# Optimization experiments

Hardware: AMD Instinct MI355X
Metric: run time of the kernel (lower is better)

## Reference

```python
import jax, jax.numpy as jnp
import numpy as np

B, S, T, H, NH, NL = 16, 128, 64, 128, 8, 4
DH = H // NH
FF = 2 * H
SCALE = 1.0 / float(np.sqrt(DH))


def _ln(x, s, b):
    m = x.mean(-1, keepdims=True)
    v = ((x - m) ** 2).mean(-1, keepdims=True)
    return (x - m) * jax.lax.rsqrt(v + 1e-5) * s + b


def _block(x, mask, p):
    Wq, bq, Wk, bk, Wv, bv, Wo, bo, s1, c1, W1, d1, W2, d2, s2, c2 = p
    N, L, _ = x.shape
    q = (x @ Wq + bq).reshape(N, L, NH, DH)
    k = (x @ Wk + bk).reshape(N, L, NH, DH)
    v = (x @ Wv + bv).reshape(N, L, NH, DH)
    scores = jnp.einsum('nqhd,nkhd->nhqk', q, k) * SCALE
    scores = jnp.where(mask[:, None, :, :], scores, -1e9)
    a = jax.nn.softmax(scores, axis=-1)
    o = jnp.einsum('nhqk,nkhd->nqhd', a, v).reshape(N, L, H)
    x = _ln(x + o @ Wo + bo, s1, c1)
    h = jax.nn.relu(x @ W1 + d1)
    return _ln(x + h @ W2 + d2, s2, c2)


def setup_inputs():
    key = jax.random.key(0)
    ks = jax.random.split(key, 16)
    g = lambda k, shape: jax.random.normal(k, shape, jnp.float32) * 0.02
    return {
        'polylines': jax.random.normal(ks[0], (B, S, T, H), jnp.float32),
        'lengths': jax.random.randint(ks[1], (B, S), 0, T + 1),
        'proj_w': g(ks[2], (H, H)), 'proj_b': jnp.zeros((H,), jnp.float32),
        'proj_ln_s': jnp.ones((H,), jnp.float32), 'proj_ln_b': jnp.zeros((H,), jnp.float32),
        'pos_emb': g(ks[3], (1, T, H)),
        'Wq': g(ks[4], (NL, H, H)), 'bq': jnp.zeros((NL, H), jnp.float32),
        'Wk': g(ks[5], (NL, H, H)), 'bk': jnp.zeros((NL, H), jnp.float32),
        'Wv': g(ks[6], (NL, H, H)), 'bv': jnp.zeros((NL, H), jnp.float32),
        'Wo': g(ks[7], (NL, H, H)), 'bo': jnp.zeros((NL, H), jnp.float32),
        'ln1_s': jnp.ones((NL, H), jnp.float32), 'ln1_b': jnp.zeros((NL, H), jnp.float32),
        'W1': g(ks[8], (NL, H, FF)), 'b1': jnp.zeros((NL, FF), jnp.float32),
        'W2': g(ks[9], (NL, FF, H)), 'b2': jnp.zeros((NL, H), jnp.float32),
        'ln2_s': jnp.ones((NL, H), jnp.float32), 'ln2_b': jnp.zeros((NL, H), jnp.float32),
    }


def reference(polylines, lengths, proj_w, proj_b, proj_ln_s, proj_ln_b, pos_emb,
              Wq, bq, Wk, bk, Wv, bv, Wo, bo, ln1_s, ln1_b, W1, b1, W2, b2, ln2_s, ln2_b):
    # valid[b,s,t] = t < lengths[b,s]; lengths==0 -> polyline absent (fully padded)
    valid = jnp.arange(T)[None, None, :] < lengths[:, :, None]  # [B,S,T]
    x = jnp.where(valid[..., None], polylines, -1.0)            # -1 pad as in np.pad(constant_values=-1)
    # mask_temporal[b,s] = outer(valid[b,s], valid[b,s])
    mask_t = (valid[:, :, :, None] & valid[:, :, None, :]).reshape(B * S, T, T)
    # mask_spatial[b,t] = outer(valid[b,:,t], valid[b,:,t])
    vs = jnp.transpose(valid, (0, 2, 1))                        # [B,T,S]
    mask_s = (vs[:, :, :, None] & vs[:, :, None, :]).reshape(B * T, S, S)

    x = x.reshape(B * S, T, H)
    x = jax.nn.relu(_ln(x @ proj_w + proj_b, proj_ln_s, proj_ln_b))  # MLP: Linear->LN->ReLU
    x = x + pos_emb[:, :T, :]

    mask = mask_t
    for i in range(NL):
        if i == NL // 2:
            # switch from temporal to spatial attention: [B*S,T,H] -> [B*T,S,H]
            x = x.reshape(B, S, T, H).transpose(0, 2, 1, 3).reshape(B * T, S, H)
            mask = mask_s
        p = (Wq[i], bq[i], Wk[i], bk[i], Wv[i], bv[i], Wo[i], bo[i],
             ln1_s[i], ln1_b[i], W1[i], b1[i], W2[i], b2[i], ln2_s[i], ln2_b[i])
        x = _block(x, mask, p)
    # faithful to original final reshape (treats [B*T,S,H] buffer as [B,S,T,H])
    return x.reshape(B, S, T, H)[:, 0, :]
```

## Files before the change

kernel.cpp:

```cpp
#include <hip/hip_runtime.h>

typedef short short8 __attribute__((ext_vector_type(8)));
typedef short short4_t __attribute__((ext_vector_type(4)));
typedef float floatx4 __attribute__((ext_vector_type(4)));
typedef unsigned short ushort_t;

#define B_ 16
#define S_ 128
#define T_ 64
#define H_ 128
#define FF_ 256
#define SCALEQK 0.25f

#define OFFP 0
#define OFFQ(l) (16384 + (l) * 65536)
#define OFFK(l) (OFFQ(l) + 16384)
#define OFFV(l) (OFFQ(l) + 32768)
#define OFFO(l) (OFFQ(l) + 49152)
#define OFFW1(l) (278528 + (l) * 65536)
#define OFFW2(l) (OFFW1(l) + 32768)

__device__ __forceinline__ float b2f(ushort_t u) {
    union { unsigned int i; float f; } x; x.i = ((unsigned int)u) << 16; return x.f;
}
__device__ __forceinline__ ushort_t f2b(float f) {
    union { float f; unsigned int i; } x; x.f = f;
    unsigned int r = x.i + 0x7fffu + ((x.i >> 16) & 1u);
    return (ushort_t)(r >> 16);
}
__device__ __forceinline__ int pack2b(float a, float b) {
    return (int)f2b(a) | ((int)f2b(b) << 16);
}

struct WtEnt { const float* src; int N; int K; int nclog2; int dstoff; };
struct WtArgs { WtEnt e[25]; };

__global__ __launch_bounds__(256) void wt_kernel(WtArgs a, ushort_t* __restrict__ dst) {
    WtEnt ent = a.e[blockIdx.x];
    const int tiles_c = ent.N >> 5;
    const int nt = (ent.K >> 5) * tiles_c;
    const int t = blockIdx.y;
    if (t >= nt) return;
    const int tc = t & (tiles_c - 1);
    const int tr = t >> ent.nclog2;
    __shared__ float ld[32 * 33];
    const int tid = threadIdx.x;
#pragma unroll
    for (int i = 0; i < 4; ++i) {
        int e = tid + i * 256;
        int rr = e >> 5, cc = e & 31;
        ld[rr * 33 + cc] = ent.src[(tr * 32 + rr) * ent.N + tc * 32 + cc];
    }
    __syncthreads();
    ushort_t* d = dst + ent.dstoff;
#pragma unroll
    for (int i = 0; i < 4; ++i) {
        int e = tid + i * 256;
        int rr = e >> 5, cc = e & 31;
        d[(tc * 32 + rr) * ent.K + tr * 32 + cc] = f2b(ld[cc * 33 + rr]);
    }
}

template<int RT, int CT, int KK>
__device__ __forceinline__ void mm_g(const ushort_t* aL, int sa,
                                     const ushort_t* __restrict__ wT,
                                     int colbase, int lane, floatx4 (&acc)[RT][CT]) {
    const int l15 = lane & 15, lq8 = (lane >> 4) * 8;
#pragma unroll
    for (int r = 0; r < RT; ++r)
#pragma unroll
        for (int c = 0; c < CT; ++c) acc[r][c] = (floatx4){0.f, 0.f, 0.f, 0.f};
#pragma unroll
    for (int k0 = 0; k0 < KK; k0 += 32) {
        short8 b[CT];
#pragma unroll
        for (int c = 0; c < CT; ++c)
            b[c] = *(const short8*)&wT[(colbase + c * 16 + l15) * KK + k0 + lq8];
#pragma unroll
        for (int r = 0; r < RT; ++r) {
            short8 a = *(const short8*)&aL[(r * 16 + l15) * sa + k0 + lq8];
#pragma unroll
            for (int c = 0; c < CT; ++c)
                acc[r][c] = __builtin_amdgcn_mfma_f32_16x16x32_bf16(a, b[c], acc[r][c], 0, 0, 0);
        }
    }
}

template<int RT, int CT>
__device__ __forceinline__ void add_bias(floatx4 (&acc)[RT][CT], const float* b,
                                         int colbase, int l15) {
#pragma unroll
    for (int c = 0; c < CT; ++c) {
        float bc = b[colbase + c * 16 + l15];
#pragma unroll
        for (int r = 0; r < RT; ++r)
#pragma unroll
            for (int g = 0; g < 4; ++g) acc[r][c][g] += bc;
    }
}

template<int RT, int CT>
__device__ __forceinline__ void add_resid_reg(floatx4 (&acc)[RT][CT],
                                              const float (&res)[RT][CT][4]) {
#pragma unroll
    for (int r = 0; r < RT; ++r)
#pragma unroll
        for (int c = 0; c < CT; ++c)
#pragma unroll
            for (int g = 0; g < 4; ++g) acc[r][c][g] += res[r][c][g];
}
template<int RT, int CT>
__device__ __forceinline__ void save_resid(float (&res)[RT][CT][4],
                                           const floatx4 (&acc)[RT][CT]) {
#pragma unroll
    for (int r = 0; r < RT; ++r)
#pragma unroll
        for (int c = 0; c < CT; ++c)
#pragma unroll
            for (int g = 0; g < 4; ++g) res[r][c][g] = acc[r][c][g];
}

template<int RT, int CT>
__device__ __forceinline__ void st_n(const floatx4 (&acc)[RT][CT], ushort_t* dst, int stride,
                                     int colbase, int l15, int lq) {
#pragma unroll
    for (int r = 0; r < RT; ++r)
#pragma unroll
        for (int g = 0; g < 4; ++g) {
            int row = r * 16 + lq * 4 + g;
#pragma unroll
            for (int c = 0; c < CT; ++c)
                dst[row * stride + colbase + c * 16 + l15] = f2b(acc[r][c][g]);
        }
}

template<int RT, int CT>
__device__ __forceinline__ void st_t(const floatx4 (&acc)[RT][CT], ushort_t* dst, int stride,
                                     int colbase, int l15, int lq) {
#pragma unroll
    for (int r = 0; r < RT; ++r)
#pragma unroll
        for (int c = 0; c < CT; ++c) {
            int d = colbase + c * 16 + l15;
            short4_t p;
#pragma unroll
            for (int g = 0; g < 4; ++g) p[g] = (short)f2b(acc[r][c][g]);
            *(short4_t*)&dst[d * stride + r * 16 + lq * 4] = p;
        }
}

template<int RT, int CT>
__device__ __forceinline__ void ln_norm(floatx4 (&acc)[RT][CT], float* redL,
                                        const float* lns, const float* lnb,
                                        int colbase, int l15, int lq, int wv) {
#pragma unroll
    for (int r = 0; r < RT; ++r)
#pragma unroll
        for (int g = 0; g < 4; ++g) {
            float s = 0.f, q = 0.f;
#pragma unroll
            for (int c = 0; c < CT; ++c) { float v = acc[r][c][g]; s += v; q += v * v; }
            s += __shfl_xor(s, 1); s += __shfl_xor(s, 2); s += __shfl_xor(s, 4); s += __shfl_xor(s, 8);
            q += __shfl_xor(q, 1); q += __shfl_xor(q, 2); q += __shfl_xor(q, 4); q += __shfl_xor(q, 8);
            if (l15 == 0) {
                int row = r * 16 + lq * 4 + g;
                redL[row * 8 + wv] = s;
                redL[row * 8 + 4 + wv] = q;
            }
        }
    __syncthreads();
#pragma unroll
    for (int r = 0; r < RT; ++r)
#pragma unroll
        for (int g = 0; g < 4; ++g) {
            int row = r * 16 + lq * 4 + g;
            float4 S = *(float4*)&redL[row * 8];
            float4 Q = *(float4*)&redL[row * 8 + 4];
            float mean = (S.x + S.y + S.z + S.w) * (1.f / 128.f);
            float var = (Q.x + Q.y + Q.z + Q.w) * (1.f / 128.f) - mean * mean;
            float rstd = rsqrtf(var + 1e-5f);
#pragma unroll
            for (int c = 0; c < CT; ++c) {
                int col = colbase + c * 16 + l15;
                acc[r][c][g] = (acc[r][c][g] - mean) * rstd * lns[col] + lnb[col];
            }
        }
}

template<int JT>
__device__ __forceinline__ void softmax_pack(floatx4 (&st)[JT], bool iv, unsigned jm,
                                             int (&px)[JT][2]) {
    float ev[JT][4];
    float mx = -3.0e38f;
#pragma unroll
    for (int jt = 0; jt < JT; ++jt)
#pragma unroll
        for (int g = 0; g < 4; ++g) {
            bool ok = iv && ((jm >> (jt * 4 + g)) & 1u);
            float s = ok ? st[jt][g] * SCALEQK : -1e9f;
            ev[jt][g] = s; mx = fmaxf(mx, s);
        }
    mx = fmaxf(mx, __shfl_xor(mx, 16)); mx = fmaxf(mx, __shfl_xor(mx, 32));
    float sum = 0.f;
#pragma unroll
    for (int jt = 0; jt < JT; ++jt)
#pragma unroll
        for (int g = 0; g < 4; ++g) { float e = __expf(ev[jt][g] - mx); ev[jt][g] = e; sum += e; }
    sum += __shfl_xor(sum, 16); sum += __shfl_xor(sum, 32);
    float inv = 1.f / sum;
#pragma unroll
    for (int jt = 0; jt < JT; ++jt) {
        px[jt][0] = pack2b(ev[jt][0] * inv, ev[jt][1] * inv);
        px[jt][1] = pack2b(ev[jt][2] * inv, ev[jt][3] * inv);
    }
}

__device__ __forceinline__ short8 pfrag(const int (*px)[2], int jc, int lq, int l15) {
    const int jA = (lq & 1) * 32 + l15;
    int a0 = __shfl(px[jc * 2][0], jA);
    int a1 = __shfl(px[jc * 2][1], jA);
    int a2 = __shfl(px[jc * 2][0], jA + 16);
    int a3 = __shfl(px[jc * 2][1], jA + 16);
    int b0 = __shfl(px[jc * 2 + 1][0], jA);
    int b1 = __shfl(px[jc * 2 + 1][1], jA);
    int b2 = __shfl(px[jc * 2 + 1][0], jA + 16);
    int b3 = __shfl(px[jc * 2 + 1][1], jA + 16);
    const bool t = (lq >> 1) != 0;
    union { int4 i; short8 s; } u;
    u.i = make_int4(t ? b0 : a0, t ? b1 : a1, t ? b2 : a2, t ? b3 : a3);
    return u.s;
}
__device__ __forceinline__ short8 vfrag(const ushort_t* vT, int stride, int row, int off) {
    int2 a = *(const int2*)&vT[row * stride + off];
    int2 b = *(const int2*)&vT[row * stride + off + 4];
    union { int4 i; short8 s; } u;
    u.i = make_int4(a.x, a.y, b.x, b.y);
    return u.s;
}

__global__ __launch_bounds__(256, 2) void k1_mega(
    const float* __restrict__ poly, const int* __restrict__ lens,
    const ushort_t* __restrict__ wt,
    const float* __restrict__ projb, const float* __restrict__ pls,
    const float* __restrict__ plb, const float* __restrict__ pos,
    const float* __restrict__ bq0, const float* __restrict__ bk0,
    const float* __restrict__ bv0, const float* __restrict__ bo0,
    const float* __restrict__ l1s0, const float* __restrict__ l1b0,
    const float* __restrict__ b10, const float* __restrict__ b20,
    const float* __restrict__ l2s0, const float* __restrict__ l2b0,
    const float* __restrict__ bq1, const float* __restrict__ bk1,
    const float* __restrict__ bv1,
    ushort_t* __restrict__ o1, float* __restrict__ xr0f)
{
    __shared__ ushort_t pool[34816];
    __shared__ float redL[512];
    __shared__ float psL[8 * 68];
    __shared__ float q1L[128];
    ushort_t* xL = pool;
    ushort_t* qL = pool + 8704;
    ushort_t* kL = pool + 17408;
    ushort_t* vT = pool + 26112;
    ushort_t* hL = pool + 17408;

    const int tid = threadIdx.x, lane = tid & 63, wv = tid >> 6;
    const int l15 = lane & 15, lq = lane >> 4;
    const int g = blockIdx.x;
    const int len = lens[g];

    {
        const float* pg = poly + (size_t)g * 8192;
#pragma unroll
        for (int it = 0; it < 8; ++it) {
            int e4 = (tid + it * 256) * 4;
            int row = e4 >> 7, col = e4 & 127;
            float4 f = *(const float4*)(pg + e4);
            if (row >= len) { f.x = -1.f; f.y = -1.f; f.z = -1.f; f.w = -1.f; }
            short4_t u;
            u[0] = (short)f2b(f.x); u[1] = (short)f2b(f.y);
            u[2] = (short)f2b(f.z); u[3] = (short)f2b(f.w);
            *(short4_t*)&xL[row * 136 + col] = u;
        }
    }
    __syncthreads();

    floatx4 a2[4][2];
    float xre[4][2][4];

    mm_g<4, 2, 128>(xL, 136, wt + OFFP, wv * 32, lane, a2);
    add_bias<4, 2>(a2, projb, wv * 32, l15);
    ln_norm<4, 2>(a2, redL, pls, plb, wv * 32, l15, lq, wv);
    __syncthreads();
#pragma unroll
    for (int r = 0; r < 4; ++r)
#pragma unroll
        for (int gg = 0; gg < 4; ++gg) {
            int row = r * 16 + lq * 4 + gg;
#pragma unroll
            for (int c = 0; c < 2; ++c) {
                int col = wv * 32 + c * 16 + l15;
                float v = fmaxf(a2[r][c][gg], 0.f) + pos[row * 128 + col];
                xre[r][c][gg] = v;
                xL[row * 136 + col] = f2b(v);
            }
        }
    __syncthreads();

    mm_g<4, 2, 128>(xL, 136, wt + OFFQ(0), wv * 32, lane, a2);
    add_bias<4, 2>(a2, bq0, wv * 32, l15);
    st_n<4, 2>(a2, qL, 136, wv * 32, l15, lq);
    mm_g<4, 2, 128>(xL, 136, wt + OFFK(0), wv * 32, lane, a2);
    add_bias<4, 2>(a2, bk0, wv * 32, l15);
    st_n<4, 2>(a2, kL, 136, wv * 32, l15, lq);
    mm_g<4, 2, 128>(xL, 136, wt + OFFV(0), wv * 32, lane, a2);
    add_bias<4, 2>(a2, bv0, wv * 32, l15);
    st_t<4, 2>(a2, vT, 68, wv * 32, l15, lq);
    __syncthreads();

    {
        const int iRow = wv * 16 + l15;
        const bool iv = iRow < len;
        unsigned jm = 0;
#pragma unroll
        for (int jt = 0; jt < 4; ++jt)
#pragma unroll
            for (int gg = 0; gg < 4; ++gg)
                if (jt * 16 + lq * 4 + gg < len) jm |= (1u << (jt * 4 + gg));
        for (int h = 0; h < 8; ++h) {
            const int hc = h * 16;
            short8 z8 = {0, 0, 0, 0, 0, 0, 0, 0};
            short8 bqf = z8;
            if (lq < 2) bqf = *(const short8*)&qL[iRow * 136 + hc + lq * 8];
            floatx4 st[4];
#pragma unroll
            for (int jt = 0; jt < 4; ++jt) {
                short8 ak = z8;
                if (lq < 2) ak = *(const short8*)&kL[(jt * 16 + l15) * 136 + hc + lq * 8];
                floatx4 zz = {0.f, 0.f, 0.f, 0.f};
                st[jt] = __builtin_amdgcn_mfma_f32_16x16x32_bf16(ak, bqf, zz, 0, 0, 0);
            }
            int px[4][2];
            softmax_pack<4>(st, iv, jm, px);
            floatx4 ao = {0.f, 0.f, 0.f, 0.f};
#pragma unroll
            for (int jc = 0; jc < 2; ++jc) {
                short8 av = vfrag(vT, 68, hc + l15, jc * 32 + lq * 8);
                short8 bp = pfrag(px, jc, lq, l15);
                ao = __builtin_amdgcn_mfma_f32_16x16x32_bf16(av, bp, ao, 0, 0, 0);
            }
            short4_t w;
#pragma unroll
            for (int gg = 0; gg < 4; ++gg) w[gg] = (short)f2b(ao[gg]);
            *(short4_t*)&qL[iRow * 136 + hc + lq * 4] = w;
        }
    }
    __syncthreads();

    mm_g<4, 2, 128>(qL, 136, wt + OFFO(0), wv * 32, lane, a2);
    add_bias<4, 2>(a2, bo0, wv * 32, l15);
    add_resid_reg<4, 2>(a2, xre);
    ln_norm<4, 2>(a2, redL, l1s0, l1b0, wv * 32, l15, lq, wv);
    save_resid<4, 2>(xre, a2);
    st_n<4, 2>(a2, xL, 136, wv * 32, l15, lq);
    __syncthreads();

    {
        floatx4 a4[4][4];
        mm_g<4, 4, 128>(xL, 136, wt + OFFW1(0), wv * 64, lane, a4);
        add_bias<4, 4>(a4, b10, wv * 64, l15);
#pragma unroll
        for (int r = 0; r < 4; ++r)
#pragma unroll
            for (int c = 0; c < 4; ++c)
#pragma unroll
                for (int gg = 0; gg < 4; ++gg) a4[r][c][gg] = fmaxf(a4[r][c][gg], 0.f);
        st_n<4, 4>(a4, hL, 272, wv * 64, l15, lq);
    }
    __syncthreads();

    mm_g<4, 2, 256>(hL, 272, wt + OFFW2(0), wv * 32, lane, a2);
    add_bias<4, 2>(a2, b20, wv * 32, l15);
    add_resid_reg<4, 2>(a2, xre);
    ln_norm<4, 2>(a2, redL, l2s0, l2b0, wv * 32, l15, lq, wv);
    save_resid<4, 2>(xre, a2);
    st_n<4, 2>(a2, xL, 136, wv * 32, l15, lq);
    if (lq == 0) {
#pragma unroll
        for (int c = 0; c < 2; ++c)
            xr0f[(size_t)g * 128 + wv * 32 + c * 16 + l15] = a2[0][c][0];
    }
    __syncthreads();

    mm_g<4, 2, 128>(xL, 136, wt + OFFK(1), wv * 32, lane, a2);
    add_bias<4, 2>(a2, bk1, wv * 32, l15);
    st_n<4, 2>(a2, kL, 136, wv * 32, l15, lq);
    mm_g<4, 2, 128>(xL, 136, wt + OFFV(1), wv * 32, lane, a2);
    add_bias<4, 2>(a2, bv1, wv * 32, l15);
    st_t<4, 2>(a2, vT, 68, wv * 32, l15, lq);
    if (tid < 128) {
        int d = tid;
        float a = bq1[d];
        const ushort_t* wq = wt + OFFQ(1) + d * 128;
#pragma unroll 4
        for (int j0 = 0; j0 < 128; j0 += 8) {
            short8 w8 = *(const short8*)&wq[j0];
            short8 x8 = *(const short8*)&xL[j0];
#pragma unroll
            for (int q = 0; q < 8; ++q)
                a = fmaf(b2f((ushort_t)x8[q]), b2f((ushort_t)w8[q]), a);
        }
        q1L[d] = a;
    }
    __syncthreads();

    {
        int h = tid >> 5, jj = tid & 31;
        int hc = h * 16;
        float s[2];
#pragma unroll
        for (int half = 0; half < 2; ++half) {
            int j = jj + half * 32;
            float a = 0.f;
            short8 k0v = *(const short8*)&kL[j * 136 + hc];
            short8 k1v = *(const short8*)&kL[j * 136 + hc + 8];
#pragma unroll
            for (int q = 0; q < 8; ++q) {
                a = fmaf(q1L[hc + q], b2f((ushort_t)k0v[q]), a);
                a = fmaf(q1L[hc + 8 + q], b2f((ushort_t)k1v[q]), a);
            }
            s[half] = (j < len) ? a * SCALEQK : -1e9f;
        }
        float mx = fmaxf(s[0], s[1]);
#pragma unroll
        for (int d = 1; d < 32; d <<= 1) mx = fmaxf(mx, __shfl_xor(mx, d));
        float e0 = __expf(s[0] - mx), e1 = __expf(s[1] - mx);
        float sum = e0 + e1;
#pragma unroll
        for (int d = 1; d < 32; d <<= 1) sum += __shfl_xor(sum, d);
        float inv = 1.f / sum;
        psL[h * 68 + jj] = e0 * inv;
        psL[h * 68 + jj + 32] = e1 * inv;
    }
    __syncthreads();
    if (tid < 128) {
        int h = tid >> 4, d = tid & 15, hc = h * 16;
        float a = 0.f;
#pragma unroll 4
        for (int j0 = 0; j0 < 64; j0 += 4) {
            float4 p4 = *(const float4*)&psL[h * 68 + j0];
            short4_t v4 = *(const short4_t*)&vT[(hc + d) * 68 + j0];
            a += p4.x * b2f((ushort_t)v4[0]) + p4.y * b2f((ushort_t)v4[1])
               + p4.z * b2f((ushort_t)v4[2]) + p4.w * b2f((ushort_t)v4[3]);
        }
        o1[(size_t)g * 128 + hc + d] = f2b(a);
    }
}

__global__ __launch_bounds__(256, 1) void k2_tail(
    const int* __restrict__ lens, const ushort_t* __restrict__ wt,
    const ushort_t* __restrict__ o1, const float* __restrict__ xr0f,
    const float* __restrict__ bq, const float* __restrict__ bk,
    const float* __restrict__ bv, const float* __restrict__ bo,
    const float* __restrict__ l1s, const float* __restrict__ l1b,
    const float* __restrict__ b1, const float* __restrict__ b2,
    const float* __restrict__ l2s, const float* __restrict__ l2b,
    float* __restrict__ outp)
{
    __shared__ ushort_t pool[69632];
    __shared__ float redL[1024];
    __shared__ int vld[128];
    ushort_t* yL = pool;
    ushort_t* qL = pool + 17408;
    ushort_t* kL = pool + 34816;
    ushort_t* vT = pool + 52224;
    ushort_t* hL = pool + 34816;

    const int tid = threadIdx.x, lane = tid & 63, wv = tid >> 6;
    const int l15 = lane & 15, lq = lane >> 4;
    const int b = blockIdx.x;

    if (tid < 128) vld[tid] = (lens[b * 128 + tid] > 0) ? 1 : 0;
#pragma unroll
    for (int it = 0; it < 8; ++it) {
        int e = tid + it * 256;
        int row = e >> 4, cg = e & 15;
        *(short8*)&kL[row * 136 + cg * 8] =
            *(const short8*)&o1[((size_t)b * 128 + row) * 128 + cg * 8];
    }
    __syncthreads();

    floatx4 a2[8][2];
    float yre[8][2][4];

    mm_g<8, 2, 128>(kL, 136, wt + OFFO(1), wv * 32, lane, a2);
    add_bias<8, 2>(a2, bo + 128, wv * 32, l15);
#pragma unroll
    for (int r = 0; r < 8; ++r)
#pragma unroll
        for (int gg = 0; gg < 4; ++gg) {
            int row = r * 16 + lq * 4 + gg;
#pragma unroll
            for (int c = 0; c < 2; ++c)
                a2[r][c][gg] += xr0f[((size_t)b * 128 + row) * 128 + wv * 32 + c * 16 + l15];
        }
    ln_norm<8, 2>(a2, redL, l1s + 128, l1b + 128, wv * 32, l15, lq, wv);
    save_resid<8, 2>(yre, a2);
    st_n<8, 2>(a2, yL, 136, wv * 32, l15, lq);
    __syncthreads();
    {
        floatx4 a4[8][4];
        mm_g<8, 4, 128>(yL, 136, wt + OFFW1(1), wv * 64, lane, a4);
        add_bias<8, 4>(a4, b1 + FF_, wv * 64, l15);
#pragma unroll
        for (int r = 0; r < 8; ++r)
#pragma unroll
            for (int c = 0; c < 4; ++c)
#pragma unroll
                for (int gg = 0; gg < 4; ++gg) a4[r][c][gg] = fmaxf(a4[r][c][gg], 0.f);
        st_n<8, 4>(a4, hL, 272, wv * 64, l15, lq);
    }
    __syncthreads();
    mm_g<8, 2, 256>(hL, 272, wt + OFFW2(1), wv * 32, lane, a2);
    add_bias<8, 2>(a2, b2 + 128, wv * 32, l15);
    add_resid_reg<8, 2>(a2, yre);
    ln_norm<8, 2>(a2, redL, l2s + 128, l2b + 128, wv * 32, l15, lq, wv);
    save_resid<8, 2>(yre, a2);
    st_n<8, 2>(a2, yL, 136, wv * 32, l15, lq);
    __syncthreads();

    unsigned jm = 0;
#pragma unroll
    for (int jt = 0; jt < 8; ++jt)
#pragma unroll
        for (int gg = 0; gg < 4; ++gg)
            if (vld[jt * 16 + lq * 4 + gg]) jm |= (1u << (jt * 4 + gg));
    const int i0 = wv * 32 + l15, i1 = i0 + 16;
    const bool iv0 = vld[i0] != 0, iv1 = vld[i1] != 0;

    for (int l = 2; l < 4; ++l) {
        mm_g<8, 2, 128>(yL, 136, wt + OFFQ(l), wv * 32, lane, a2);
        add_bias<8, 2>(a2, bq + l * 128, wv * 32, l15);
        st_n<8, 2>(a2, qL, 136, wv * 32, l15, lq);
        mm_g<8, 2, 128>(yL, 136, wt + OFFK(l), wv * 32, lane, a2);
        add_bias<8, 2>(a2, bk + l * 128, wv * 32, l15);
        st_n<8, 2>(a2, kL, 136, wv * 32, l15, lq);
        mm_g<8, 2, 128>(yL, 136, wt + OFFV(l), wv * 32, lane, a2);
        add_bias<8, 2>(a2, bv + l * 128, wv * 32, l15);
        st_t<8, 2>(a2, vT, 136, wv * 32, l15, lq);
        __syncthreads();
        for (int h = 0; h < 8; ++h) {
            const int hc = h * 16;
            short8 z8 = {0, 0, 0, 0, 0, 0, 0, 0};
            short8 bqa = z8, bqb = z8;
            if (lq < 2) {
                bqa = *(const short8*)&qL[i0 * 136 + hc + lq * 8];
                bqb = *(const short8*)&qL[i1 * 136 + hc + lq * 8];
            }
            floatx4 s0[8], s1[8];
#pragma unroll
            for (int jt = 0; jt < 8; ++jt) {
                short8 ak = z8;
                if (lq < 2) ak = *(const short8*)&kL[(jt * 16 + l15) * 136 + hc + lq * 8];
                floatx4 zz = {0.f, 0.f, 0.f, 0.f};
                s0[jt] = __builtin_amdgcn_mfma_f32_16x16x32_bf16(ak, bqa, zz, 0, 0, 0);
                s1[jt] = __builtin_amdgcn_mfma_f32_16x16x32_bf16(ak, bqb, zz, 0, 0, 0);
            }
            int px0[8][2], px1[8][2];
            softmax_pack<8>(s0, iv0, jm, px0);
            softmax_pack<8>(s1, iv1, jm, px1);
            floatx4 o0 = {0.f, 0.f, 0.f, 0.f}, o1a = {0.f, 0.f, 0.f, 0.f};
#pragma unroll
            for (int jc = 0; jc < 4; ++jc) {
                short8 av = vfrag(vT, 136, hc + l15, jc * 32 + lq * 8);
                o0 = __builtin_amdgcn_mfma_f32_16x16x32_bf16(av, pfrag(px0, jc, lq, l15), o0, 0, 0, 0);
                o1a = __builtin_amdgcn_mfma_f32_16x16x32_bf16(av, pfrag(px1, jc, lq, l15), o1a, 0, 0, 0);
            }
            short4_t w0, w1;
#pragma unroll
            for (int gg = 0; gg < 4; ++gg) { w0[gg] = (short)f2b(o0[gg]); w1[gg] = (short)f2b(o1a[gg]); }
            *(short4_t*)&qL[i0 * 136 + hc + lq * 4] = w0;
            *(short4_t*)&qL[i1 * 136 + hc + lq * 4] = w1;
        }
        __syncthreads();
        mm_g<8, 2, 128>(qL, 136, wt + OFFO(l), wv * 32, lane, a2);
        add_bias<8, 2>(a2, bo + l * 128, wv * 32, l15);
        add_resid_reg<8, 2>(a2, yre);
        ln_norm<8, 2>(a2, redL, l1s + l * 128, l1b + l * 128, wv * 32, l15, lq, wv);
        save_resid<8, 2>(yre, a2);
        st_n<8, 2>(a2, yL, 136, wv * 32, l15, lq);
        __syncthreads();
        {
            floatx4 a4[8][4];
            mm_g<8, 4, 128>(yL, 136, wt + OFFW1(l), wv * 64, lane, a4);
            add_bias<8, 4>(a4, b1 + l * FF_, wv * 64, l15);
#pragma unroll
            for (int r = 0; r < 8; ++r)
#pragma unroll
                for (int c = 0; c < 4; ++c)
#pragma unroll
                    for (int gg = 0; gg < 4; ++gg) a4[r][c][gg] = fmaxf(a4[r][c][gg], 0.f);
            st_n<8, 4>(a4, hL, 272, wv * 64, l15, lq);
        }
        __syncthreads();
        mm_g<8, 2, 256>(hL, 272, wt + OFFW2(l), wv * 32, lane, a2);
        add_bias<8, 2>(a2, b2 + l * 128, wv * 32, l15);
        add_resid_reg<8, 2>(a2, yre);
        ln_norm<8, 2>(a2, redL, l2s + l * 128, l2b + l * 128, wv * 32, l15, lq, wv);
        if (l == 3) {
#pragma unroll
            for (int r = 0; r < 4; ++r)
#pragma unroll
                for (int gg = 0; gg < 4; ++gg) {
                    int row = r * 16 + lq * 4 + gg;
#pragma unroll
                    for (int c = 0; c < 2; ++c)
                        outp[(size_t)b * 8192 + row * 128 + wv * 32 + c * 16 + l15] = a2[r][c][gg];
                }
        } else {
            save_resid<8, 2>(yre, a2);
            st_n<8, 2>(a2, yL, 136, wv * 32, l15, lq);
        }
        __syncthreads();
    }
}

extern "C" void kernel_launch(void* const* d_in, const int* in_sizes, int n_in,
                              void* d_out, int out_size, void* d_ws, size_t ws_size,
                              hipStream_t stream)
{
    const float* poly   = (const float*)d_in[0];
    const int*   lens   = (const int*)d_in[1];
    const float* proj_w = (const float*)d_in[2];
    const float* proj_b = (const float*)d_in[3];
    const float* pls    = (const float*)d_in[4];
    const float* plb    = (const float*)d_in[5];
    const float* pos    = (const float*)d_in[6];
    const float* Wq = (const float*)d_in[7];
    const float* bq = (const float*)d_in[8];
    const float* Wk = (const float*)d_in[9];
    const float* bk = (const float*)d_in[10];
    const float* Wv = (const float*)d_in[11];
    const float* bv = (const float*)d_in[12];
    const float* Wo = (const float*)d_in[13];
    const float* bo = (const float*)d_in[14];
    const float* l1s = (const float*)d_in[15];
    const float* l1b = (const float*)d_in[16];
    const float* W1 = (const float*)d_in[17];
    const float* b1 = (const float*)d_in[18];
    const float* W2 = (const float*)d_in[19];
    const float* b2 = (const float*)d_in[20];
    const float* l2s = (const float*)d_in[21];
    const float* l2b = (const float*)d_in[22];
    float* outp = (float*)d_out;

    char* base = (char*)d_ws;
    ushort_t* wt    = (ushort_t*)base;
    ushort_t* o1buf = (ushort_t*)(base + 1081344);
    float* xr0f     = (float*)(base + 1605632);

    const int HH = H_ * H_, HF = H_ * FF_;
    WtArgs wa;
    wa.e[0] = {proj_w, 128, 128, 2, OFFP};
    for (int l = 0; l < 4; ++l) {
        wa.e[1 + l * 4 + 0] = {Wq + l * HH, 128, 128, 2, OFFQ(l)};
        wa.e[1 + l * 4 + 1] = {Wk + l * HH, 128, 128, 2, OFFK(l)};
        wa.e[1 + l * 4 + 2] = {Wv + l * HH, 128, 128, 2, OFFV(l)};
        wa.e[1 + l * 4 + 3] = {Wo + l * HH, 128, 128, 2, OFFO(l)};
    }
    for (int l = 0; l < 4; ++l) {
        wa.e[17 + l * 2 + 0] = {W1 + l * HF, 256, 128, 3, OFFW1(l)};
        wa.e[17 + l * 2 + 1] = {W2 + l * HF, 128, 256, 2, OFFW2(l)};
    }
    wt_kernel<<<dim3(25, 32), 256, 0, stream>>>(wa, wt);

    k1_mega<<<dim3(2048), 256, 0, stream>>>(
        poly, lens, wt,
        proj_b, pls, plb, pos,
        bq, bk, bv, bo, l1s, l1b, b1, b2, l2s, l2b,
        bq + H_, bk + H_, bv + H_,
        o1buf, xr0f);

    k2_tail<<<dim3(16), 256, 0, stream>>>(
        lens, wt, o1buf, xr0f,
        bq, bk, bv, bo, l1s, l1b, b1, b2, l2s, l2b,
        outp);
}
```

Baseline: 471.6 us.

## Move layer-1 Wo/LN/FFN tail from 16-block k2 into 2048-block k1

The layer-1 output projection, first layernorm, FFN and second layernorm for the single needed row (t=0) are now computed per polyline inside k1_mega using scalar dot products over bf16 weights, and written as fp32 to a buffer. k2_tail, which runs only 16 blocks, no longer performs these three matmuls and two layernorms over 128 rows; it just loads the finished activations. This spreads serial tail work across many blocks, at the cost of extra per-block latency and weight reads in k1.

```diff
diff --git a/kernel.cpp b/kernel.cpp
--- a/kernel.cpp
+++ b/kernel.cpp
@@ -249,13 +249,17 @@
     const float* __restrict__ b10, const float* __restrict__ b20,
     const float* __restrict__ l2s0, const float* __restrict__ l2b0,
     const float* __restrict__ bq1, const float* __restrict__ bk1,
-    const float* __restrict__ bv1,
-    ushort_t* __restrict__ o1, float* __restrict__ xr0f)
+    const float* __restrict__ bv1, const float* __restrict__ bo1,
+    const float* __restrict__ l1s1, const float* __restrict__ l1b1,
+    const float* __restrict__ b11, const float* __restrict__ b21,
+    const float* __restrict__ l2s1, const float* __restrict__ l2b1,
+    float* __restrict__ ybuf)
 {
     __shared__ ushort_t pool[34816];
     __shared__ float redL[512];
     __shared__ float psL[8 * 68];
     __shared__ float q1L[128];
+    __shared__ float x0L[128];
     ushort_t* xL = pool;
     ushort_t* qL = pool + 8704;
     ushort_t* kL = pool + 17408;
@@ -264,11 +268,11 @@
 
     const int tid = threadIdx.x, lane = tid & 63, wv = tid >> 6;
     const int l15 = lane & 15, lq = lane >> 4;
-    const int g = blockIdx.x;
-    const int len = lens[g];
+    const int gid = blockIdx.x;
+    const int len = lens[gid];
 
     {
-        const float* pg = poly + (size_t)g * 8192;
+        const float* pg = poly + (size_t)gid * 8192;
 #pragma unroll
         for (int it = 0; it < 8; ++it) {
             int e4 = (tid + it * 256) * 4;
@@ -386,7 +390,7 @@
     if (lq == 0) {
 #pragma unroll
         for (int c = 0; c < 2; ++c)
-            xr0f[(size_t)g * 128 + wv * 32 + c * 16 + l15] = a2[0][c][0];
+            x0L[wv * 32 + c * 16 + l15] = a2[0][c][0];
     }
     __syncthreads();
 
@@ -451,13 +455,85 @@
             a += p4.x * b2f((ushort_t)v4[0]) + p4.y * b2f((ushort_t)v4[1])
                + p4.z * b2f((ushort_t)v4[2]) + p4.w * b2f((ushort_t)v4[3]);
         }
-        o1[(size_t)g * 128 + hc + d] = f2b(a);
+        q1L[tid] = a;
+    }
+    __syncthreads();
+
+    float accv = 0.f;
+    if (tid < 128) {
+        accv = bo1[tid] + x0L[tid];
+        const ushort_t* wrow = wt + OFFO(1) + tid * 128;
+#pragma unroll 4
+        for (int j0 = 0; j0 < 128; j0 += 8) {
+            short8 w8 = *(const short8*)&wrow[j0];
+#pragma unroll
+            for (int q = 0; q < 8; ++q)
+                accv = fmaf(q1L[j0 + q], b2f((ushort_t)w8[q]), accv);
+        }
+    }
+    {
+        float s = accv, q = accv * accv;
+        s += __shfl_xor(s, 1); s += __shfl_xor(s, 2); s += __shfl_xor(s, 4);
+        s += __shfl_xor(s, 8); s += __shfl_xor(s, 16); s += __shfl_xor(s, 32);
+        q += __shfl_xor(q, 1); q += __shfl_xor(q, 2); q += __shfl_xor(q, 4);
+        q += __shfl_xor(q, 8); q += __shfl_xor(q, 16); q += __shfl_xor(q, 32);
+        if (lane == 0 && wv < 2) { redL[wv] = s; redL[2 + wv] = q; }
+    }
+    __syncthreads();
+    if (tid < 128) {
+        float s = redL[0] + redL[1], q = redL[2] + redL[3];
+        float mean = s * (1.f / 128.f);
+        float rstd = rsqrtf(q * (1.f / 128.f) - mean * mean + 1e-5f);
+        q1L[tid] = (accv - mean) * rstd * l1s1[tid] + l1b1[tid];
+    }
+    __syncthreads();
+
+    {
+        float hh = b11[tid];
+        const ushort_t* wrow = wt + OFFW1(1) + tid * 128;
+#pragma unroll 4
+        for (int j0 = 0; j0 < 128; j0 += 8) {
+            short8 w8 = *(const short8*)&wrow[j0];
+#pragma unroll
+            for (int q = 0; q < 8; ++q)
+                hh = fmaf(q1L[j0 + q], b2f((ushort_t)w8[q]), hh);
+        }
+        psL[tid] = fmaxf(hh, 0.f);
+    }
+    __syncthreads();
+
+    accv = 0.f;
+    if (tid < 128) {
+        accv = b21[tid] + q1L[tid];
+        const ushort_t* wrow = wt + OFFW2(1) + tid * 256;
+#pragma unroll 4
+        for (int j0 = 0; j0 < 256; j0 += 8) {
+            short8 w8 = *(const short8*)&wrow[j0];
+#pragma unroll
+            for (int q = 0; q < 8; ++q)
+                accv = fmaf(psL[j0 + q], b2f((ushort_t)w8[q]), accv);
+        }
+    }
+    {
+        float s = accv, q = accv * accv;
+        s += __shfl_xor(s, 1); s += __shfl_xor(s, 2); s += __shfl_xor(s, 4);
+        s += __shfl_xor(s, 8); s += __shfl_xor(s, 16); s += __shfl_xor(s, 32);
+        q += __shfl_xor(q, 1); q += __shfl_xor(q, 2); q += __shfl_xor(q, 4);
+        q += __shfl_xor(q, 8); q += __shfl_xor(q, 16); q += __shfl_xor(q, 32);
+        if (lane == 0 && wv < 2) { redL[4 + wv] = s; redL[6 + wv] = q; }
+    }
+    __syncthreads();
+    if (tid < 128) {
+        float s = redL[4] + redL[5], q = redL[6] + redL[7];
+        float mean = s * (1.f / 128.f);
+        float rstd = rsqrtf(q * (1.f / 128.f) - mean * mean + 1e-5f);
+        ybuf[(size_t)gid * 128 + tid] = (accv - mean) * rstd * l2s1[tid] + l2b1[tid];
     }
 }
 
 __global__ __launch_bounds__(256, 1) void k2_tail(
     const int* __restrict__ lens, const ushort_t* __restrict__ wt,
-    const ushort_t* __restrict__ o1, const float* __restrict__ xr0f,
+    const float* __restrict__ ybuf,
     const float* __restrict__ bq, const float* __restrict__ bk,
     const float* __restrict__ bv, const float* __restrict__ bo,
     const float* __restrict__ l1s, const float* __restrict__ l1b,
@@ -479,52 +555,23 @@
     const int b = blockIdx.x;
 
     if (tid < 128) vld[tid] = (lens[b * 128 + tid] > 0) ? 1 : 0;
-#pragma unroll
-    for (int it = 0; it < 8; ++it) {
-        int e = tid + it * 256;
-        int row = e >> 4, cg = e & 15;
-        *(short8*)&kL[row * 136 + cg * 8] =
-            *(const short8*)&o1[((size_t)b * 128 + row) * 128 + cg * 8];
-    }
-    __syncthreads();
 
     floatx4 a2[8][2];
     float yre[8][2][4];
 
-    mm_g<8, 2, 128>(kL, 136, wt + OFFO(1), wv * 32, lane, a2);
-    add_bias<8, 2>(a2, bo + 128, wv * 32, l15);
 #pragma unroll
     for (int r = 0; r < 8; ++r)
 #pragma unroll
         for (int gg = 0; gg < 4; ++gg) {
             int row = r * 16 + lq * 4 + gg;
 #pragma unroll
-            for (int c = 0; c < 2; ++c)
-                a2[r][c][gg] += xr0f[((size_t)b * 128 + row) * 128 + wv * 32 + c * 16 + l15];
-        }
-    ln_norm<8, 2>(a2, redL, l1s + 128, l1b + 128, wv * 32, l15, lq, wv);
-    save_resid<8, 2>(yre, a2);
-    st_n<8, 2>(a2, yL, 136, wv * 32, l15, lq);
-    __syncthreads();
-    {
-        floatx4 a4[8][4];
-        mm_g<8, 4, 128>(yL, 136, wt + OFFW1(1), wv * 64, lane, a4);
-        add_bias<8, 4>(a4, b1 + FF_, wv * 64, l15);
-#pragma unroll
-        for (int r = 0; r < 8; ++r)
-#pragma unroll
-            for (int c = 0; c < 4; ++c)
-#pragma unroll
-                for (int gg = 0; gg < 4; ++gg) a4[r][c][gg] = fmaxf(a4[r][c][gg], 0.f);
-        st_n<8, 4>(a4, hL, 272, wv * 64, l15, lq);
-    }
-    __syncthreads();
-    mm_g<8, 2, 256>(hL, 272, wt + OFFW2(1), wv * 32, lane, a2);
-    add_bias<8, 2>(a2, b2 + 128, wv * 32, l15);
-    add_resid_reg<8, 2>(a2, yre);
-    ln_norm<8, 2>(a2, redL, l2s + 128, l2b + 128, wv * 32, l15, lq, wv);
-    save_resid<8, 2>(yre, a2);
-    st_n<8, 2>(a2, yL, 136, wv * 32, l15, lq);
+            for (int c = 0; c < 2; ++c) {
+                int col = wv * 32 + c * 16 + l15;
+                float v = ybuf[((size_t)b * 128 + row) * 128 + col];
+                yre[r][c][gg] = v;
+                yL[row * 136 + col] = f2b(v);
+            }
+        }
     __syncthreads();
 
     unsigned jm = 0;
@@ -653,9 +700,8 @@
     float* outp = (float*)d_out;
 
     char* base = (char*)d_ws;
-    ushort_t* wt    = (ushort_t*)base;
-    ushort_t* o1buf = (ushort_t*)(base + 1081344);
-    float* xr0f     = (float*)(base + 1605632);
+    ushort_t* wt = (ushort_t*)base;
+    float* ybuf  = (float*)(base + 1081344);
 
     const int HH = H_ * H_, HF = H_ * FF_;
     WtArgs wa;
@@ -676,11 +722,12 @@
         poly, lens, wt,
         proj_b, pls, plb, pos,
         bq, bk, bv, bo, l1s, l1b, b1, b2, l2s, l2b,
-        bq + H_, bk + H_, bv + H_,
-        o1buf, xr0f);
+        bq + H_, bk + H_, bv + H_, bo + H_,
+        l1s + H_, l1b + H_, b1 + FF_, b2 + H_, l2s + H_, l2b + H_,
+        ybuf);
 
     k2_tail<<<dim3(16), 256, 0, stream>>>(
-        lens, wt, o1buf, xr0f,
+        lens, wt, ybuf,
         bq, bk, bv, bo, l1s, l1b, b1, b2, l2s, l2b,
         outp);
 }
```

New measurement: 486.7 us. +3.2%, slower.

## Double k2_tail block to 512 threads, one head per wave in attention

Applied to the files above, without the earlier changes.

The tail kernel runs only 16 blocks, so it now uses 8 waves per block instead of 4. Each wave owns 16 output columns in the projections and FFN, and exactly one attention head. The LayerNorm reduction is templated on wave count so cross-wave partial sums cover 8 waves. This is meant to cut the latency of the serial tail kernel, at the cost of more registers per block and more LDS reduction traffic.

```diff
diff --git a/kernel.cpp b/kernel.cpp
--- a/kernel.cpp
+++ b/kernel.cpp
@@ -149,7 +149,7 @@
         }
 }
 
-template<int RT, int CT>
+template<int RT, int CT, int NW>
 __device__ __forceinline__ void ln_norm(floatx4 (&acc)[RT][CT], float* redL,
                                         const float* lns, const float* lnb,
                                         int colbase, int l15, int lq, int wv) {
@@ -164,8 +164,8 @@
             q += __shfl_xor(q, 1); q += __shfl_xor(q, 2); q += __shfl_xor(q, 4); q += __shfl_xor(q, 8);
             if (l15 == 0) {
                 int row = r * 16 + lq * 4 + g;
-                redL[row * 8 + wv] = s;
-                redL[row * 8 + 4 + wv] = q;
+                redL[row * 2 * NW + wv] = s;
+                redL[row * 2 * NW + NW + wv] = q;
             }
         }
     __syncthreads();
@@ -174,10 +174,16 @@
 #pragma unroll
         for (int g = 0; g < 4; ++g) {
             int row = r * 16 + lq * 4 + g;
-            float4 S = *(float4*)&redL[row * 8];
-            float4 Q = *(float4*)&redL[row * 8 + 4];
-            float mean = (S.x + S.y + S.z + S.w) * (1.f / 128.f);
-            float var = (Q.x + Q.y + Q.z + Q.w) * (1.f / 128.f) - mean * mean;
+            float s = 0.f, q = 0.f;
+#pragma unroll
+            for (int w8 = 0; w8 < NW; w8 += 4) {
+                float4 S = *(float4*)&redL[row * 2 * NW + w8];
+                float4 Q = *(float4*)&redL[row * 2 * NW + NW + w8];
+                s += S.x + S.y + S.z + S.w;
+                q += Q.x + Q.y + Q.z + Q.w;
+            }
+            float mean = s * (1.f / 128.f);
+            float var = q * (1.f / 128.f) - mean * mean;
             float rstd = rsqrtf(var + 1e-5f);
 #pragma unroll
             for (int c = 0; c < CT; ++c) {
@@ -264,11 +270,11 @@
 
     const int tid = threadIdx.x, lane = tid & 63, wv = tid >> 6;
     const int l15 = lane & 15, lq = lane >> 4;
-    const int g = blockIdx.x;
-    const int len = lens[g];
+    const int gid = blockIdx.x;
+    const int len = lens[gid];
 
     {
-        const float* pg = poly + (size_t)g * 8192;
+        const float* pg = poly + (size_t)gid * 8192;
 #pragma unroll
         for (int it = 0; it < 8; ++it) {
             int e4 = (tid + it * 256) * 4;
@@ -288,7 +294,7 @@
 
     mm_g<4, 2, 128>(xL, 136, wt + OFFP, wv * 32, lane, a2);
     add_bias<4, 2>(a2, projb, wv * 32, l15);
-    ln_norm<4, 2>(a2, redL, pls, plb, wv * 32, l15, lq, wv);
+    ln_norm<4, 2, 4>(a2, redL, pls, plb, wv * 32, l15, lq, wv);
     __syncthreads();
 #pragma unroll
     for (int r = 0; r < 4; ++r)
@@ -358,7 +364,7 @@
     mm_g<4, 2, 128>(qL, 136, wt + OFFO(0), wv * 32, lane, a2);
     add_bias<4, 2>(a2, bo0, wv * 32, l15);
     add_resid_reg<4, 2>(a2, xre);
-    ln_norm<4, 2>(a2, redL, l1s0, l1b0, wv * 32, l15, lq, wv);
+    ln_norm<4, 2, 4>(a2, redL, l1s0, l1b0, wv * 32, l15, lq, wv);
     save_resid<4, 2>(xre, a2);
     st_n<4, 2>(a2, xL, 136, wv * 32, l15, lq);
     __syncthreads();
@@ -380,13 +386,13 @@
     mm_g<4, 2, 256>(hL, 272, wt + OFFW2(0), wv * 32, lane, a2);
     add_bias<4, 2>(a2, b20, wv * 32, l15);
     add_resid_reg<4, 2>(a2, xre);
-    ln_norm<4, 2>(a2, redL, l2s0, l2b0, wv * 32, l15, lq, wv);
+    ln_norm<4, 2, 4>(a2, redL, l2s0, l2b0, wv * 32, l15, lq, wv);
     save_resid<4, 2>(xre, a2);
     st_n<4, 2>(a2, xL, 136, wv * 32, l15, lq);
     if (lq == 0) {
 #pragma unroll
         for (int c = 0; c < 2; ++c)
-            xr0f[(size_t)g * 128 + wv * 32 + c * 16 + l15] = a2[0][c][0];
+            xr0f[(size_t)gid * 128 + wv * 32 + c * 16 + l15] = a2[0][c][0];
     }
     __syncthreads();
 
@@ -451,11 +457,11 @@
             a += p4.x * b2f((ushort_t)v4[0]) + p4.y * b2f((ushort_t)v4[1])
                + p4.z * b2f((ushort_t)v4[2]) + p4.w * b2f((ushort_t)v4[3]);
         }
-        o1[(size_t)g * 128 + hc + d] = f2b(a);
-    }
-}
-
-__global__ __launch_bounds__(256, 1) void k2_tail(
+        o1[(size_t)gid * 128 + hc + d] = f2b(a);
+    }
+}
+
+__global__ __launch_bounds__(512, 1) void k2_tail(
     const int* __restrict__ lens, const ushort_t* __restrict__ wt,
     const ushort_t* __restrict__ o1, const float* __restrict__ xr0f,
     const float* __restrict__ bq, const float* __restrict__ bk,
@@ -466,7 +472,7 @@
     float* __restrict__ outp)
 {
     __shared__ ushort_t pool[69632];
-    __shared__ float redL[1024];
+    __shared__ float redL[2048];
     __shared__ int vld[128];
     ushort_t* yL = pool;
     ushort_t* qL = pool + 17408;
@@ -477,54 +483,54 @@
     const int tid = threadIdx.x, lane = tid & 63, wv = tid >> 6;
     const int l15 = lane & 15, lq = lane >> 4;
     const int b = blockIdx.x;
+    const int cb1 = wv * 16;
+    const int cb2 = wv * 32;
 
     if (tid < 128) vld[tid] = (lens[b * 128 + tid] > 0) ? 1 : 0;
 #pragma unroll
-    for (int it = 0; it < 8; ++it) {
-        int e = tid + it * 256;
+    for (int it = 0; it < 4; ++it) {
+        int e = tid + it * 512;
         int row = e >> 4, cg = e & 15;
         *(short8*)&kL[row * 136 + cg * 8] =
             *(const short8*)&o1[((size_t)b * 128 + row) * 128 + cg * 8];
     }
     __syncthreads();
 
-    floatx4 a2[8][2];
-    float yre[8][2][4];
-
-    mm_g<8, 2, 128>(kL, 136, wt + OFFO(1), wv * 32, lane, a2);
-    add_bias<8, 2>(a2, bo + 128, wv * 32, l15);
+    floatx4 a1[8][1];
+    float yre[8][1][4];
+
+    mm_g<8, 1, 128>(kL, 136, wt + OFFO(1), cb1, lane, a1);
+    add_bias<8, 1>(a1, bo + 128, cb1, l15);
 #pragma unroll
     for (int r = 0; r < 8; ++r)
 #pragma unroll
         for (int gg = 0; gg < 4; ++gg) {
             int row = r * 16 + lq * 4 + gg;
+            a1[r][0][gg] += xr0f[((size_t)b * 128 + row) * 128 + cb1 + l15];
+        }
+    ln_norm<8, 1, 8>(a1, redL, l1s + 128, l1b + 128, cb1, l15, lq, wv);
+    save_resid<8, 1>(yre, a1);
+    st_n<8, 1>(a1, yL, 136, cb1, l15, lq);
+    __syncthreads();
+    {
+        floatx4 aw[8][2];
+        mm_g<8, 2, 128>(yL, 136, wt + OFFW1(1), cb2, lane, aw);
+        add_bias<8, 2>(aw, b1 + FF_, cb2, l15);
+#pragma unroll
+        for (int r = 0; r < 8; ++r)
 #pragma unroll
             for (int c = 0; c < 2; ++c)
-                a2[r][c][gg] += xr0f[((size_t)b * 128 + row) * 128 + wv * 32 + c * 16 + l15];
-        }
-    ln_norm<8, 2>(a2, redL, l1s + 128, l1b + 128, wv * 32, l15, lq, wv);
-    save_resid<8, 2>(yre, a2);
-    st_n<8, 2>(a2, yL, 136, wv * 32, l15, lq);
-    __syncthreads();
-    {
-        floatx4 a4[8][4];
-        mm_g<8, 4, 128>(yL, 136, wt + OFFW1(1), wv * 64, lane, a4);
-        add_bias<8, 4>(a4, b1 + FF_, wv * 64, l15);
-#pragma unroll
-        for (int r = 0; r < 8; ++r)
-#pragma unroll
-            for (int c = 0; c < 4; ++c)
-#pragma unroll
-                for (int gg = 0; gg < 4; ++gg) a4[r][c][gg] = fmaxf(a4[r][c][gg], 0.f);
-        st_n<8, 4>(a4, hL, 272, wv * 64, l15, lq);
-    }
-    __syncthreads();
-    mm_g<8, 2, 256>(hL, 272, wt + OFFW2(1), wv * 32, lane, a2);
-    add_bias<8, 2>(a2, b2 + 128, wv * 32, l15);
-    add_resid_reg<8, 2>(a2, yre);
-    ln_norm<8, 2>(a2, redL, l2s + 128, l2b + 128, wv * 32, l15, lq, wv);
-    save_resid<8, 2>(yre, a2);
-    st_n<8, 2>(a2, yL, 136, wv * 32, l15, lq);
+#pragma unroll
+                for (int gg = 0; gg < 4; ++gg) aw[r][c][gg] = fmaxf(aw[r][c][gg], 0.f);
+        st_n<8, 2>(aw, hL, 272, cb2, l15, lq);
+    }
+    __syncthreads();
+    mm_g<8, 1, 256>(hL, 272, wt + OFFW2(1), cb1, lane, a1);
+    add_bias<8, 1>(a1, b2 + 128, cb1, l15);
+    add_resid_reg<8, 1>(a1, yre);
+    ln_norm<8, 1, 8>(a1, redL, l2s + 128, l2b + 128, cb1, l15, lq, wv);
+    save_resid<8, 1>(yre, a1);
+    st_n<8, 1>(a1, yL, 136, cb1, l15, lq);
     __syncthreads();
 
     unsigned jm = 0;
@@ -533,91 +539,92 @@
 #pragma unroll
         for (int gg = 0; gg < 4; ++gg)
             if (vld[jt * 16 + lq * 4 + gg]) jm |= (1u << (jt * 4 + gg));
-    const int i0 = wv * 32 + l15, i1 = i0 + 16;
-    const bool iv0 = vld[i0] != 0, iv1 = vld[i1] != 0;
 
     for (int l = 2; l < 4; ++l) {
-        mm_g<8, 2, 128>(yL, 136, wt + OFFQ(l), wv * 32, lane, a2);
-        add_bias<8, 2>(a2, bq + l * 128, wv * 32, l15);
-        st_n<8, 2>(a2, qL, 136, wv * 32, l15, lq);
-        mm_g<8, 2, 128>(yL, 136, wt + OFFK(l), wv * 32, lane, a2);
-        add_bias<8, 2>(a2, bk + l * 128, wv * 32, l15);
-        st_n<8, 2>(a2, kL, 136, wv * 32, l15, lq);
-        mm_g<8, 2, 128>(yL, 136, wt + OFFV(l), wv * 32, lane, a2);
-        add_bias<8, 2>(a2, bv + l * 128, wv * 32, l15);
-        st_t<8, 2>(a2, vT, 136, wv * 32, l15, lq);
-        __syncthreads();
-        for (int h = 0; h < 8; ++h) {
-            const int hc = h * 16;
-            short8 z8 = {0, 0, 0, 0, 0, 0, 0, 0};
-            short8 bqa = z8, bqb = z8;
-            if (lq < 2) {
-                bqa = *(const short8*)&qL[i0 * 136 + hc + lq * 8];
-                bqb = *(const short8*)&qL[i1 * 136 + hc + lq * 8];
-            }
-            floatx4 s0[8], s1[8];
-#pragma unroll
-            for (int jt = 0; jt < 8; ++jt) {
-                short8 ak = z8;
-                if (lq < 2) ak = *(const short8*)&kL[(jt * 16 + l15) * 136 + hc + lq * 8];
-                floatx4 zz = {0.f, 0.f, 0.f, 0.f};
-                s0[jt] = __builtin_amdgcn_mfma_f32_16x16x32_bf16(ak, bqa, zz, 0, 0, 0);
-                s1[jt] = __builtin_amdgcn_mfma_f32_16x16x32_bf16(ak, bqb, zz, 0, 0, 0);
-            }
-            int px0[8][2], px1[8][2];
-            softmax_pack<8>(s0, iv0, jm, px0);
-            softmax_pack<8>(s1, iv1, jm, px1);
-            floatx4 o0 = {0.f, 0.f, 0.f, 0.f}, o1a = {0.f, 0.f, 0.f, 0.f};
-#pragma unroll
-            for (int jc = 0; jc < 4; ++jc) {
-                short8 av = vfrag(vT, 136, hc + l15, jc * 32 + lq * 8);
-                o0 = __builtin_amdgcn_mfma_f32_16x16x32_bf16(av, pfrag(px0, jc, lq, l15), o0, 0, 0, 0);
-                o1a = __builtin_amdgcn_mfma_f32_16x16x32_bf16(av, pfrag(px1, jc, lq, l15), o1a, 0, 0, 0);
-            }
-            short4_t w0, w1;
-#pragma unroll
-            for (int gg = 0; gg < 4; ++gg) { w0[gg] = (short)f2b(o0[gg]); w1[gg] = (short)f2b(o1a[gg]); }
-            *(short4_t*)&qL[i0 * 136 + hc + lq * 4] = w0;
-            *(short4_t*)&qL[i1 * 136 + hc + lq * 4] = w1;
-        }
-        __syncthreads();
-        mm_g<8, 2, 128>(qL, 136, wt + OFFO(l), wv * 32, lane, a2);
-        add_bias<8, 2>(a2, bo + l * 128, wv * 32, l15);
-        add_resid_reg<8, 2>(a2, yre);
-        ln_norm<8, 2>(a2, redL, l1s + l * 128, l1b + l * 128, wv * 32, l15, lq, wv);
-        save_resid<8, 2>(yre, a2);
-        st_n<8, 2>(a2, yL, 136, wv * 32, l15, lq);
+        mm_g<8, 1, 128>(yL, 136, wt + OFFQ(l), cb1, lane, a1);
+        add_bias<8, 1>(a1, bq + l * 128, cb1, l15);
+        st_n<8, 1>(a1, qL, 136, cb1, l15, lq);
+        mm_g<8, 1, 128>(yL, 136, wt + OFFK(l), cb1, lane, a1);
+        add_bias<8, 1>(a1, bk + l * 128, cb1, l15);
+        st_n<8, 1>(a1, kL, 136, cb1, l15, lq);
+        mm_g<8, 1, 128>(yL, 136, wt + OFFV(l), cb1, lane, a1);
+        add_bias<8, 1>(a1, bv + l * 128, cb1, l15);
+        st_t<8, 1>(a1, vT, 136, cb1, l15, lq);
         __syncthreads();
         {
-            floatx4 a4[8][4];
-            mm_g<8, 4, 128>(yL, 136, wt + OFFW1(l), wv * 64, lane, a4);
-            add_bias<8, 4>(a4, b1 + l * FF_, wv * 64, l15);
+            const int hc = wv * 16;
+#pragma unroll
+            for (int it = 0; it < 4; ++it) {
+                const int i0 = it * 32 + l15, i1 = i0 + 16;
+                const bool iv0 = vld[i0] != 0, iv1 = vld[i1] != 0;
+                short8 z8 = {0, 0, 0, 0, 0, 0, 0, 0};
+                short8 bqa = z8, bqb = z8;
+                if (lq < 2) {
+                    bqa = *(const short8*)&qL[i0 * 136 + hc + lq * 8];
+                    bqb = *(const short8*)&qL[i1 * 136 + hc + lq * 8];
+                }
+                floatx4 s0[8], s1[8];
+#pragma unroll
+                for (int jt = 0; jt < 8; ++jt) {
+                    short8 ak = z8;
+                    if (lq < 2) ak = *(const short8*)&kL[(jt * 16 + l15) * 136 + hc + lq * 8];
+                    floatx4 zz = {0.f, 0.f, 0.f, 0.f};
+                    s0[jt] = __builtin_amdgcn_mfma_f32_16x16x32_bf16(ak, bqa, zz, 0, 0, 0);
+                    s1[jt] = __builtin_amdgcn_mfma_f32_16x16x32_bf16(ak, bqb, zz, 0, 0, 0);
+                }
+                int px0[8][2], px1[8][2];
+                softmax_pack<8>(s0, iv0, jm, px0);
+                softmax_pack<8>(s1, iv1, jm, px1);
+                floatx4 o0 = {0.f, 0.f, 0.f, 0.f}, o1a = {0.f, 0.f, 0.f, 0.f};
+#pragma unroll
+                for (int jc = 0; jc < 4; ++jc) {
+                    short8 av = vfrag(vT, 136, hc + l15, jc * 32 + lq * 8);
+                    o0 = __builtin_amdgcn_mfma_f32_16x16x32_bf16(av, pfrag(px0, jc, lq, l15), o0, 0, 0, 0);
+                    o1a = __builtin_amdgcn_mfma_f32_16x16x32_bf16(av, pfrag(px1, jc, lq, l15), o1a, 0, 0, 0);
+                }
+                short4_t w0, w1;
+#pragma unroll
+                for (int gg = 0; gg < 4; ++gg) { w0[gg] = (short)f2b(o0[gg]); w1[gg] = (short)f2b(o1a[gg]); }
+                *(short4_t*)&qL[i0 * 136 + hc + lq * 4] = w0;
+                *(short4_t*)&qL[i1 * 136 + hc + lq * 4] = w1;
+            }
+        }
+        __syncthreads();
+        mm_g<8, 1, 128>(qL, 136, wt + OFFO(l), cb1, lane, a1);
+        add_bias<8, 1>(a1, bo + l * 128, cb1, l15);
+        add_resid_reg<8, 1>(a1, yre);
+        ln_norm<8, 1, 8>(a1, redL, l1s + l * 128, l1b + l * 128, cb1, l15, lq, wv);
+        save_resid<8, 1>(yre, a1);
+        st_n<8, 1>(a1, yL, 136, cb1, l15, lq);
+        __syncthreads();
+        {
+            floatx4 aw[8][2];
+            mm_g<8, 2, 128>(yL, 136, wt + OFFW1(l), cb2, lane, aw);
+            add_bias<8, 2>(aw, b1 + l * FF_, cb2, l15);
 #pragma unroll
             for (int r = 0; r < 8; ++r)
 #pragma unroll
-                for (int c = 0; c < 4; ++c)
-#pragma unroll
-                    for (int gg = 0; gg < 4; ++gg) a4[r][c][gg] = fmaxf(a4[r][c][gg], 0.f);
-            st_n<8, 4>(a4, hL, 272, wv * 64, l15, lq);
+                for (int c = 0; c < 2; ++c)
+#pragma unroll
+                    for (int gg = 0; gg < 4; ++gg) aw[r][c][gg] = fmaxf(aw[r][c][gg], 0.f);
+            st_n<8, 2>(aw, hL, 272, cb2, l15, lq);
         }
         __syncthreads();
-        mm_g<8, 2, 256>(hL, 272, wt + OFFW2(l), wv * 32, lane, a2);
-        add_bias<8, 2>(a2, b2 + l * 128, wv * 32, l15);
-        add_resid_reg<8, 2>(a2, yre);
-        ln_norm<8, 2>(a2, redL, l2s + l * 128, l2b + l * 128, wv * 32, l15, lq, wv);
+        mm_g<8, 1, 256>(hL, 272, wt + OFFW2(l), cb1, lane, a1);
+        add_bias<8, 1>(a1, b2 + l * 128, cb1, l15);
+        add_resid_reg<8, 1>(a1, yre);
+        ln_norm<8, 1, 8>(a1, redL, l2s + l * 128, l2b + l * 128, cb1, l15, lq, wv);
         if (l == 3) {
 #pragma unroll
             for (int r = 0; r < 4; ++r)
 #pragma unroll
                 for (int gg = 0; gg < 4; ++gg) {
                     int row = r * 16 + lq * 4 + gg;
-#pragma unroll
-                    for (int c = 0; c < 2; ++c)
-                        outp[(size_t)b * 8192 + row * 128 + wv * 32 + c * 16 + l15] = a2[r][c][gg];
+                    outp[(size_t)b * 8192 + row * 128 + cb1 + l15] = a1[r][0][gg];
                 }
         } else {
-            save_resid<8, 2>(yre, a2);
-            st_n<8, 2>(a2, yL, 136, wv * 32, l15, lq);
+            save_resid<8, 1>(yre, a1);
+            st_n<8, 1>(a1, yL, 136, cb1, l15, lq);
         }
         __syncthreads();
     }
@@ -679,7 +686,7 @@
         bq + H_, bk + H_, bv + H_,
         o1buf, xr0f);
 
-    k2_tail<<<dim3(16), 256, 0, stream>>>(
+    k2_tail<<<dim3(16), 512, 0, stream>>>(
         lens, wt, o1buf, xr0f,
         bq, bk, bv, bo, l1s, l1b, b1, b2, l2s, l2b,
         outp);
```

Result: slower. 640.0 us (+35.7%).
